# Optimization experiments

Measured on AMD Instinct MI355X. Metric: run time of the kernel, lower is better.

## Reference

```python
import jax, jax.numpy as jnp
import numpy as np

B, L, D, H = 2, 4096, 128, 4


def setup_inputs() -> dict:
    key = jax.random.key(0)
    k_x, k_q, k_k, k_v, k_o = jax.random.split(key, 5)
    std = 0.02
    x = jax.random.normal(k_x, (B, L, D), dtype=jnp.float32)
    # torch nn.Linear(d_model, H*d_model).weight has shape [H*D, D]
    Wq = std * jax.random.normal(k_q, (H * D, D), dtype=jnp.float32)
    Wk = std * jax.random.normal(k_k, (H * D, D), dtype=jnp.float32)
    Wv = std * jax.random.normal(k_v, (H * D, D), dtype=jnp.float32)
    # W_O: Linear(H*d_model, d_model).weight -> [D, H*D]
    Wo = std * jax.random.normal(k_o, (D, H * D), dtype=jnp.float32)
    return {"x": x, "Wq": Wq, "Wk": Wk, "Wv": Wv, "Wo": Wo}


def reference(x, Wq, Wk, Wv, Wo):
    # project: weight rows indexed by (h, e); out = x @ W^T
    Wq3 = Wq.reshape(H, D, D)
    Wk3 = Wk.reshape(H, D, D)
    Wv3 = Wv.reshape(H, D, D)
    q = jnp.einsum('bld,hed->bhle', x, Wq3)  # [B,H,L,D]
    k = jnp.einsum('bld,hed->bhle', x, Wk3)
    v = jnp.einsum('bld,hed->bhle', x, Wv3)
    logits = jnp.einsum('bhle,bhme->bhlm', q, k)  # [B,H,L,L]
    causal_mask = jnp.triu(jnp.ones((L, L), dtype=bool), 1)
    neg = jnp.finfo(logits.dtype).min
    logits = jnp.where(causal_mask, neg, logits)
    attn = jax.nn.softmax(logits, axis=-1)
    ctx = jnp.einsum('bhlm,bhme->bhle', attn, v)  # [B,H,L,D]
    ctx = ctx.transpose(0, 2, 1, 3).reshape(B, L, H * D)
    y = ctx @ Wo.T  # [B,L,D]
    return y
```

## Files before the change

### kernel.cpp

```cpp
#include <hip/hip_runtime.h>
#include <hip/hip_bf16.h>

#define BB 2
#define LL 4096
#define DD 128
#define HH 4

typedef unsigned short u16;
typedef unsigned int u32;
typedef __attribute__((ext_vector_type(8))) short short8;
typedef __attribute__((ext_vector_type(4))) float floatx4;

union PFrag { short8 s; u32 u[4]; };

__device__ __forceinline__ u16 f2bf(float f) {
    union { float f; u32 u; } v; v.f = f;
    return (u16)((v.u + 0x7fffu + ((v.u >> 16) & 1u)) >> 16);
}

__device__ __forceinline__ float bf2f(u16 u) {
    union { u32 u; float f; } v; v.u = (u32)u << 16;
    return v.f;
}

__device__ __forceinline__ u32 pk2bf(float a, float b) {
    union { __hip_bfloat162 h; u32 u; } v;
    v.h = __float22bfloat162_rn(float2{a, b});
    return v.u;
}

__device__ __forceinline__ void gld16(const u16* g, u16* l) {
    __builtin_amdgcn_global_load_lds((const __attribute__((address_space(1))) void*)g,
                                     (__attribute__((address_space(3))) void*)l, 16, 0, 0);
}

__device__ __forceinline__ int pfx2(int t) {
    int a = t >> 2, b = t & 3;
    return 2 * a * (a - 1) + a * b;
}

__device__ __forceinline__ void stage_tile_f32(const float* __restrict__ g,
                                               u16* lds, int tid) {
#pragma unroll
    for (int it = 0; it < 8; it++) {
        int unit = it * 256 + tid;
        int row = unit >> 4, uu = unit & 15;
        const float4* gp = (const float4*)(g + (size_t)row * 128 + uu * 8);
        float4 f0 = gp[0], f1 = gp[1];
        PFrag pv;
        pv.u[0] = pk2bf(f0.x, f0.y); pv.u[1] = pk2bf(f0.z, f0.w);
        pv.u[2] = pk2bf(f1.x, f1.y); pv.u[3] = pk2bf(f1.z, f1.w);
        *(short8*)(&lds[row * 128 + ((uu ^ (row & 15)) * 8)]) = pv.s;
    }
}

__global__ __launch_bounds__(256) void proj_qkv(const float* __restrict__ x,
                                                const float* __restrict__ wq,
                                                const float* __restrict__ wk,
                                                const float* __restrict__ wv,
                                                u16* __restrict__ Qb,
                                                u16* __restrict__ Kb,
                                                u16* __restrict__ Vt) {
    __shared__ __align__(16) u16 At[128 * 128];
    __shared__ __align__(16) u16 Wt[2][128 * 128];
    int tid  = threadIdx.x;
    int lane = tid & 63;
    int w    = tid >> 6;
    int c = lane & 15, g = lane >> 4;
    int mt = blockIdx.x;
    int h  = blockIdx.y;

    stage_tile_f32(x  + (size_t)mt * 128 * 128, At,    tid);
    stage_tile_f32(wq + (size_t)h  * 128 * 128, Wt[0], tid);
    __syncthreads();

#pragma unroll
    for (int z = 0; z < 3; z++) {
        if (z == 0) stage_tile_f32(wk + (size_t)h * 128 * 128, Wt[1], tid);
        if (z == 1) stage_tile_f32(wv + (size_t)h * 128 * 128, Wt[0], tid);
        const u16* Wcur = Wt[z & 1];
        const u16* Abuf = (z < 2) ? At : Wcur;
        const u16* Bbuf = (z < 2) ? Wcur : At;

        floatx4 acc[2][8];
#pragma unroll
        for (int m2 = 0; m2 < 2; m2++)
#pragma unroll
            for (int n2 = 0; n2 < 8; n2++) acc[m2][n2] = (floatx4){0.f, 0.f, 0.f, 0.f};

#pragma unroll
        for (int kk = 0; kk < 4; kk++) {
            short8 a0, a1, bf[8];
            {
                int r0 = w * 32 + c;
                int r1 = r0 + 16;
                a0 = *(const short8*)(&Abuf[r0 * 128 + (((g + 4 * kk) ^ (r0 & 15)) * 8)]);
                a1 = *(const short8*)(&Abuf[r1 * 128 + (((g + 4 * kk) ^ (r1 & 15)) * 8)]);
            }
#pragma unroll
            for (int n2 = 0; n2 < 8; n2++) {
                int rn = n2 * 16 + c;
                bf[n2] = *(const short8*)(&Bbuf[rn * 128 + (((g + 4 * kk) ^ (rn & 15)) * 8)]);
            }
#pragma unroll
            for (int n2 = 0; n2 < 8; n2++) {
                acc[0][n2] = __builtin_amdgcn_mfma_f32_16x16x32_bf16(a0, bf[n2], acc[0][n2], 0, 0, 0);
                acc[1][n2] = __builtin_amdgcn_mfma_f32_16x16x32_bf16(a1, bf[n2], acc[1][n2], 0, 0, 0);
            }
        }

        if (z < 2) {
            u16* out = (z == 0) ? Qb : Kb;
#pragma unroll
            for (int m2 = 0; m2 < 2; m2++)
#pragma unroll
                for (int r = 0; r < 4; r++) {
                    int lg = mt * 128 + w * 32 + m2 * 16 + g * 4 + r;
                    int b_ = lg >> 12, l = lg & 4095;
                    u16* op = out + ((size_t)(b_ * HH + h) * LL + l) * DD + c;
#pragma unroll
                    for (int n2 = 0; n2 < 8; n2++) op[n2 * 16] = f2bf(acc[m2][n2][r]);
                }
        } else {
            int b_ = mt >> 5;
            int lbase = (mt & 31) * 128;
#pragma unroll
            for (int m2 = 0; m2 < 2; m2++)
#pragma unroll
                for (int r = 0; r < 4; r++) {
                    int e = w * 32 + m2 * 16 + g * 4 + r;
                    u16* op = Vt + ((size_t)(b_ * HH + h) * DD + e) * LL + lbase + c;
#pragma unroll
                    for (int n2 = 0; n2 < 8; n2++) op[n2 * 16] = f2bf(acc[m2][n2][r]);
                }
        }
        __syncthreads();
    }
}

__global__ __launch_bounds__(256, 3) void flash_attn(const u16* __restrict__ Q,
                                                     const u16* __restrict__ K,
                                                     const u16* __restrict__ Vt,
                                                     u16* __restrict__ basep,
                                                     u16* __restrict__ slots,
                                                     float* __restrict__ l_acc) {
    __shared__ __align__(16) u16 Kls[2][32 * 128];
    __shared__ __align__(16) u16 Vls[2][512 * 8];

    int lane = threadIdx.x & 63;
    int w    = threadIdx.x >> 6;
    int c = lane & 15, g = lane >> 4;

    int bid  = blockIdx.x;
    int head = bid & 7;
    int i    = bid >> 3;
    int t, ch;
    if (i < 120) {
        int rem = i; ch = 0;
        while (rem >= 29 - 4 * ch) { rem -= 29 - 4 * ch; ch++; }
        t = 31 - rem;
    } else {
        int j = i - 120;
        if (j < 8)       { t = 30 - 4 * j;        ch = (t - 2) >> 2; }
        else if (j < 16) { t = 29 - 4 * (j - 8);  ch = (t - 1) >> 2; }
        else             { t = 28 - 4 * (j - 16); ch = t >> 2; }
    }

    int kstart = ch << 9;
    int kend   = min((t + 1) << 7, kstart + 512);
    int nsteps = (kend - kstart) >> 5;

    int qb = t * 128 + w * 32;
    int my_steps = min(nsteps, ((qb + 31 - kstart) >> 5) + 1);

    short8 bq0[4], bq1[4];
    {
        const u16* qp0 = Q + ((size_t)head * LL + qb + c) * DD + g * 8;
        const u16* qp1 = qp0 + 16 * DD;
#pragma unroll
        for (int kk = 0; kk < 4; kk++) {
            bq0[kk] = *(const short8*)(qp0 + kk * 32);
            bq1[kk] = *(const short8*)(qp1 + kk * 32);
        }
    }

    floatx4 o0[8], o1[8];
#pragma unroll
    for (int tt = 0; tt < 8; tt++) {
        o0[tt] = (floatx4){0.f, 0.f, 0.f, 0.f};
        o1[tt] = (floatx4){0.f, 0.f, 0.f, 0.f};
    }
    float lsum0 = 0.f, lsum1 = 0.f;

    int s0 = c + (((g << 1) & 3) << 4);
    int s1 = c + ((((g << 1) | 1) & 3) << 4);
    bool hi = (g >= 2);

    const u16* Kg0 = K  + ((size_t)head * LL + kstart) * DD;
    const u16* Vg0 = Vt + (size_t)head * DD * LL + kstart;

    int q0 = w * 64 + lane;
    int r0 = q0 >> 4, cc0 = (q0 & 15) ^ (r0 & 15);
    int r1 = r0 + 16,  cc1 = (q0 & 15) ^ (r1 & 15);
    int ve  = q0 & 127;
    int vka = (q0 >> 7) * 8;

#define STAGE(s) {                                                          \
        int buf_ = (s) & 1; int kb_ = (s) << 5;                             \
        const u16* Kg = Kg0 + (size_t)kb_ * DD;                             \
        const u16* Vg = Vg0 + kb_;                                          \
        gld16(Kg + r0 * DD + cc0 * 8, &Kls[buf_][w * 512]);                 \
        gld16(Kg + r1 * DD + cc1 * 8, &Kls[buf_][2048 + w * 512]);          \
        gld16(Vg + (size_t)ve * LL + vka,      &Vls[buf_][w * 512]);        \
        gld16(Vg + (size_t)ve * LL + vka + 16, &Vls[buf_][2048 + w * 512]); \
    }

    STAGE(0);

    for (int j = 0; j < nsteps; ++j) {
        __syncthreads();
        if (j + 1 < nsteps) STAGE(j + 1);
        if (j < my_steps) {
            int kb = kstart + (j << 5);
            const u16* Kb_ = &Kls[j & 1][0];
            const u16* Vb_ = &Vls[j & 1][0];

            floatx4 st00 = {0,0,0,0}, st01 = {0,0,0,0};
            floatx4 st10 = {0,0,0,0}, st11 = {0,0,0,0};
            {
                short8 ka[4];
#pragma unroll
                for (int kk = 0; kk < 4; kk++)
                    ka[kk] = *(const short8*)(Kb_ + c * 128 + (((g + 4 * kk) ^ c)) * 8);
#pragma unroll
                for (int kk = 0; kk < 4; kk++) {
                    st00 = __builtin_amdgcn_mfma_f32_16x16x32_bf16(ka[kk], bq0[kk], st00, 0, 0, 0);
                    st10 = __builtin_amdgcn_mfma_f32_16x16x32_bf16(ka[kk], bq1[kk], st10, 0, 0, 0);
                }
#pragma unroll
                for (int kk = 0; kk < 4; kk++)
                    ka[kk] = *(const short8*)(Kb_ + (16 + c) * 128 + (((g + 4 * kk) ^ c)) * 8);
#pragma unroll
                for (int kk = 0; kk < 4; kk++) {
                    st01 = __builtin_amdgcn_mfma_f32_16x16x32_bf16(ka[kk], bq0[kk], st01, 0, 0, 0);
                    st11 = __builtin_amdgcn_mfma_f32_16x16x32_bf16(ka[kk], bq1[kk], st11, 0, 0, 0);
                }
            }

            PFrag au0, au1;
#pragma unroll
            for (int qh = 0; qh < 2; qh++) {
                floatx4 sa = qh ? st10 : st00;
                floatx4 sb = qh ? st11 : st01;
                int qbh = qb + qh * 16;
                float p[8];
                if (kb + 31 > qbh) {
                    int q_c = qbh + c;
#pragma unroll
                    for (int r = 0; r < 4; r++) {
                        int k0 = kb + g * 4 + r;
                        p[r]     = (k0      <= q_c) ? sa[r] : -INFINITY;
                        p[4 + r] = (k0 + 16 <= q_c) ? sb[r] : -INFINITY;
                    }
                } else {
#pragma unroll
                    for (int r = 0; r < 4; r++) { p[r] = sa[r]; p[4 + r] = sb[r]; }
                }
                float ls = 0.f;
#pragma unroll
                for (int i2 = 0; i2 < 8; i2++) { p[i2] = __expf(p[i2]); ls += p[i2]; }
                if (qh) lsum1 += ls; else lsum0 += ls;

                u32 pk00 = pk2bf(p[0], p[1]);
                u32 pk01 = pk2bf(p[2], p[3]);
                u32 pk10 = pk2bf(p[4], p[5]);
                u32 pk11 = pk2bf(p[6], p[7]);
                u32 x00 = (u32)__shfl((int)pk00, s0), x10 = (u32)__shfl((int)pk10, s0);
                u32 x01 = (u32)__shfl((int)pk01, s0), x11 = (u32)__shfl((int)pk11, s0);
                u32 y00 = (u32)__shfl((int)pk00, s1), y10 = (u32)__shfl((int)pk10, s1);
                u32 y01 = (u32)__shfl((int)pk01, s1), y11 = (u32)__shfl((int)pk11, s1);
                PFrag* au = qh ? &au1 : &au0;
                au->u[0] = hi ? x10 : x00;
                au->u[1] = hi ? x11 : x01;
                au->u[2] = hi ? y10 : y00;
                au->u[3] = hi ? y11 : y01;
            }

#pragma unroll
            for (int tt = 0; tt < 8; tt++) {
                short8 vb = *(const short8*)(Vb_ + g * 1024 + tt * 128 + c * 8);
                o0[tt] = __builtin_amdgcn_mfma_f32_16x16x32_bf16(au0.s, vb, o0[tt], 0, 0, 0);
                o1[tt] = __builtin_amdgcn_mfma_f32_16x16x32_bf16(au1.s, vb, o1[tt], 0, 0, 0);
            }
        }
    }
#undef STAGE

    lsum0 += __shfl_xor(lsum0, 16); lsum0 += __shfl_xor(lsum0, 32);
    lsum1 += __shfl_xor(lsum1, 16); lsum1 += __shfl_xor(lsum1, 32);
    if (g == 0) {
        atomicAdd(&l_acc[head * LL + qb + c],      lsum0);
        atomicAdd(&l_acc[head * LL + qb + 16 + c], lsum1);
    }

    bool diag = (kstart + 512 >= ((t + 1) << 7));
    u16* dst0 = diag ? basep + ((size_t)head * LL + t * 128) * 128
                     : slots + ((size_t)(head * 112 + pfx2(t) + ch)) * 16384;
    dst0 += (size_t)(w * 32) * 128;
#pragma unroll
    for (int r = 0; r < 4; r++) {
        u16* d0 = dst0 + (g * 4 + r) * 128 + c;
        u16* d1 = d0 + 16 * 128;
#pragma unroll
        for (int tt = 0; tt < 8; tt++) {
            d0[tt * 16] = f2bf(o0[tt][r]);
            d1[tt * 16] = f2bf(o1[tt][r]);
        }
    }
}

__global__ __launch_bounds__(256) void norm_cast(const u16* __restrict__ basep,
                                                 const u16* __restrict__ slots,
                                                 const float* __restrict__ l_acc,
                                                 u16* __restrict__ ctx) {
    int i = blockIdx.x * 256 + threadIdx.x;
    int e4 = i * 4;
    int col = e4 & 511;
    int bl  = e4 >> 9;
    int b_ = bl >> 12, l = bl & 4095;
    int h = col >> 7, d = col & 127;
    int head = b_ * HH + h;
    int t = l >> 7;
    int nx = t >> 2;

    ushort4 bv = *(const ushort4*)(basep + ((size_t)head * LL + l) * 128 + d);
    float v0 = bf2f(bv.x), v1 = bf2f(bv.y), v2 = bf2f(bv.z), v3 = bf2f(bv.w);
    if (nx > 0) {
        int sb = head * 112 + pfx2(t);
        for (int x = 0; x < nx; x++) {
            ushort4 sv = *(const ushort4*)(slots + (size_t)(sb + x) * 16384 + (l & 127) * 128 + d);
            v0 += bf2f(sv.x); v1 += bf2f(sv.y); v2 += bf2f(sv.z); v3 += bf2f(sv.w);
        }
    }
    float inv = 1.f / l_acc[head * LL + l];
    ushort4 o;
    o.x = f2bf(v0 * inv); o.y = f2bf(v1 * inv);
    o.z = f2bf(v2 * inv); o.w = f2bf(v3 * inv);
    *(ushort4*)(ctx + e4) = o;
}

__global__ __launch_bounds__(256) void proj_out(const u16* __restrict__ ctx,
                                                const float* __restrict__ wo,
                                                float* __restrict__ y) {
    __shared__ __align__(16) u16 At[2][128 * 64];
    __shared__ __align__(16) u16 Wt[2][128 * 64];
    int tid  = threadIdx.x;
    int lane = tid & 63;
    int w    = tid >> 6;
    int c = lane & 15, g = lane >> 4;
    int mt = blockIdx.x;
    const u16* Ag = ctx + (size_t)mt * 128 * 512;

#define PSTAGE(kc) {                                                        \
        int buf_ = (kc) & 1; int ks_ = (kc) * 64;                           \
        _Pragma("unroll")                                                   \
        for (int i = 0; i < 4; i++) {                                       \
            int row = i * 32 + w * 8 + (lane >> 3);                         \
            int cc  = (lane & 7) ^ (row & 7);                               \
            gld16(Ag + (size_t)row * 512 + ks_ + cc * 8,                    \
                  &At[buf_][(i * 32 + w * 8) * 64]);                        \
        }                                                                   \
        _Pragma("unroll")                                                   \
        for (int it = 0; it < 4; it++) {                                    \
            int unit = it * 256 + tid;                                      \
            int row = unit >> 3, uu = unit & 7;                             \
            const float4* gp = (const float4*)(wo + (size_t)row * 512 +     \
                                               ks_ + uu * 8);               \
            float4 f0 = gp[0], f1 = gp[1];                                  \
            PFrag pv;                                                       \
            pv.u[0] = pk2bf(f0.x, f0.y); pv.u[1] = pk2bf(f0.z, f0.w);       \
            pv.u[2] = pk2bf(f1.x, f1.y); pv.u[3] = pk2bf(f1.z, f1.w);       \
            *(short8*)(&Wt[buf_][row * 64 + ((uu ^ (row & 7)) * 8)]) = pv.s;\
        }                                                                   \
    }

    floatx4 acc[2][8];
#pragma unroll
    for (int m2 = 0; m2 < 2; m2++)
#pragma unroll
        for (int n2 = 0; n2 < 8; n2++) acc[m2][n2] = (floatx4){0.f, 0.f, 0.f, 0.f};

    PSTAGE(0);
    for (int kc = 0; kc < 8; kc++) {
        __syncthreads();
        if (kc + 1 < 8) PSTAGE(kc + 1);
        int buf = kc & 1;
#pragma unroll
        for (int kk = 0; kk < 2; kk++) {
            int G = g + 4 * kk;
            short8 a0, a1, bf[8];
            {
                int ra = w * 32 + c;
                int rb = ra + 16;
                a0 = *(const short8*)(&At[buf][ra * 64 + ((G ^ (ra & 7)) * 8)]);
                a1 = *(const short8*)(&At[buf][rb * 64 + ((G ^ (rb & 7)) * 8)]);
            }
#pragma unroll
            for (int n2 = 0; n2 < 8; n2++) {
                int rn = n2 * 16 + c;
                bf[n2] = *(const short8*)(&Wt[buf][rn * 64 + ((G ^ (rn & 7)) * 8)]);
            }
#pragma unroll
            for (int n2 = 0; n2 < 8; n2++) {
                acc[0][n2] = __builtin_amdgcn_mfma_f32_16x16x32_bf16(a0, bf[n2], acc[0][n2], 0, 0, 0);
                acc[1][n2] = __builtin_amdgcn_mfma_f32_16x16x32_bf16(a1, bf[n2], acc[1][n2], 0, 0, 0);
            }
        }
    }
#undef PSTAGE

#pragma unroll
    for (int m2 = 0; m2 < 2; m2++)
#pragma unroll
        for (int r = 0; r < 4; r++) {
            int m = mt * 128 + w * 32 + m2 * 16 + g * 4 + r;
            float* yp = y + (size_t)m * 128 + c;
#pragma unroll
            for (int n2 = 0; n2 < 8; n2++) yp[n2 * 16] = acc[m2][n2][r];
        }
}

extern "C" void kernel_launch(void* const* d_in, const int* in_sizes, int n_in,
                              void* d_out, int out_size, void* d_ws, size_t ws_size,
                              hipStream_t stream) {
    const float* x  = (const float*)d_in[0];
    const float* Wq = (const float*)d_in[1];
    const float* Wk = (const float*)d_in[2];
    const float* Wv = (const float*)d_in[3];
    const float* Wo = (const float*)d_in[4];
    float* y = (float*)d_out;

    u16* ws  = (u16*)d_ws;
    u16* Qb  = ws;
    u16* Kb  = Qb + (size_t)BB * HH * LL * DD;
    u16* Vt  = Kb + (size_t)BB * HH * LL * DD;
    u16* ctx = Vt + (size_t)BB * HH * LL * DD;
    u16* basep = ctx + (size_t)BB * LL * HH * DD;
    u16* slots = basep + (size_t)8 * LL * 128;
    float* l_acc = (float*)(slots + (size_t)896 * 16384);

    (void)hipMemsetAsync(l_acc, 0, (size_t)8 * LL * 4, stream);

    proj_qkv<<<dim3(64, 4), 256, 0, stream>>>(x, Wq, Wk, Wv, Qb, Kb, Vt);
    flash_attn<<<dim3(1152), 256, 0, stream>>>(Qb, Kb, Vt, basep, slots, l_acc);
    norm_cast<<<dim3(4096), 256, 0, stream>>>(basep, slots, l_acc, ctx);
    proj_out<<<dim3(64), 256, 0, stream>>>(ctx, Wo, y);
}
```

Baseline: 153.6 us.

## Halve attention key-chunk size and proj_out row tile for more blocks

The flash-attention split-K chunk shrinks from 512 to 256 keys, raising the grid from 1152 to 2176 blocks. The slot indexing (pfxB), the diagonal test and the workspace size are updated to match. Separately, proj_out now uses 64-row tiles, giving 128 blocks instead of 64. Both changes aim to fill more CUs and balance the causal workload better. In exchange, norm_cast must read and sum twice as many bf16 partial slots per row, which adds memory traffic and per-block startup cost.

```diff
diff --git a/kernel.cpp b/kernel.cpp
--- a/kernel.cpp
+++ b/kernel.cpp
@@ -34,9 +34,9 @@
                                      (__attribute__((address_space(3))) void*)l, 16, 0, 0);
 }
 
-__device__ __forceinline__ int pfx2(int t) {
-    int a = t >> 2, b = t & 3;
-    return 2 * a * (a - 1) + a * b;
+__device__ __forceinline__ int pfxB(int t) {
+    int a = t >> 1, b = t & 1;
+    return a * (a - 1) + a * b;
 }
 
 __device__ __forceinline__ void stage_tile_f32(const float* __restrict__ g,
@@ -155,19 +155,17 @@
     int head = bid & 7;
     int i    = bid >> 3;
     int t, ch;
-    if (i < 120) {
-        int rem = i; ch = 0;
-        while (rem >= 29 - 4 * ch) { rem -= 29 - 4 * ch; ch++; }
-        t = 31 - rem;
+    if (i < 240) {
+        int rem = i; t = 31;
+        while (rem >= (t >> 1)) { rem -= (t >> 1); t--; }
+        ch = rem;
     } else {
-        int j = i - 120;
-        if (j < 8)       { t = 30 - 4 * j;        ch = (t - 2) >> 2; }
-        else if (j < 16) { t = 29 - 4 * (j - 8);  ch = (t - 1) >> 2; }
-        else             { t = 28 - 4 * (j - 16); ch = t >> 2; }
-    }
-
-    int kstart = ch << 9;
-    int kend   = min((t + 1) << 7, kstart + 512);
+        t = 31 - (i - 240);
+        ch = t >> 1;
+    }
+
+    int kstart = ch << 8;
+    int kend   = min((t + 1) << 7, kstart + 256);
     int nsteps = (kend - kstart) >> 5;
 
     int qb = t * 128 + w * 32;
@@ -303,9 +301,9 @@
         atomicAdd(&l_acc[head * LL + qb + 16 + c], lsum1);
     }
 
-    bool diag = (kstart + 512 >= ((t + 1) << 7));
+    bool diag = (ch == (t >> 1));
     u16* dst0 = diag ? basep + ((size_t)head * LL + t * 128) * 128
-                     : slots + ((size_t)(head * 112 + pfx2(t) + ch)) * 16384;
+                     : slots + ((size_t)(head * 240 + pfxB(t) + ch)) * 16384;
     dst0 += (size_t)(w * 32) * 128;
 #pragma unroll
     for (int r = 0; r < 4; r++) {
@@ -331,12 +329,12 @@
     int h = col >> 7, d = col & 127;
     int head = b_ * HH + h;
     int t = l >> 7;
-    int nx = t >> 2;
+    int nx = t >> 1;
 
     ushort4 bv = *(const ushort4*)(basep + ((size_t)head * LL + l) * 128 + d);
     float v0 = bf2f(bv.x), v1 = bf2f(bv.y), v2 = bf2f(bv.z), v3 = bf2f(bv.w);
     if (nx > 0) {
-        int sb = head * 112 + pfx2(t);
+        int sb = head * 240 + pfxB(t);
         for (int x = 0; x < nx; x++) {
             ushort4 sv = *(const ushort4*)(slots + (size_t)(sb + x) * 16384 + (l & 127) * 128 + d);
             v0 += bf2f(sv.x); v1 += bf2f(sv.y); v2 += bf2f(sv.z); v3 += bf2f(sv.w);
@@ -352,23 +350,24 @@
 __global__ __launch_bounds__(256) void proj_out(const u16* __restrict__ ctx,
                                                 const float* __restrict__ wo,
                                                 float* __restrict__ y) {
-    __shared__ __align__(16) u16 At[2][128 * 64];
+    __shared__ __align__(16) u16 At[2][64 * 64];
     __shared__ __align__(16) u16 Wt[2][128 * 64];
     int tid  = threadIdx.x;
     int lane = tid & 63;
     int w    = tid >> 6;
     int c = lane & 15, g = lane >> 4;
     int mt = blockIdx.x;
-    const u16* Ag = ctx + (size_t)mt * 128 * 512;
+    const u16* Ag = ctx + (size_t)mt * 64 * 512;
 
 #define PSTAGE(kc) {                                                        \
         int buf_ = (kc) & 1; int ks_ = (kc) * 64;                           \
         _Pragma("unroll")                                                   \
-        for (int i = 0; i < 4; i++) {                                       \
-            int row = i * 32 + w * 8 + (lane >> 3);                         \
-            int cc  = (lane & 7) ^ (row & 7);                               \
+        for (int it = 0; it < 2; it++) {                                    \
+            int unit = it * 256 + tid;                                      \
+            int row = unit >> 3, uu = unit & 7;                             \
+            int cc  = uu ^ (row & 7);                                       \
             gld16(Ag + (size_t)row * 512 + ks_ + cc * 8,                    \
-                  &At[buf_][(i * 32 + w * 8) * 64]);                        \
+                  &At[buf_][it * 2048 + w * 512]);                          \
         }                                                                   \
         _Pragma("unroll")                                                   \
         for (int it = 0; it < 4; it++) {                                    \
@@ -384,11 +383,9 @@
         }                                                                   \
     }
 
-    floatx4 acc[2][8];
-#pragma unroll
-    for (int m2 = 0; m2 < 2; m2++)
-#pragma unroll
-        for (int n2 = 0; n2 < 8; n2++) acc[m2][n2] = (floatx4){0.f, 0.f, 0.f, 0.f};
+    floatx4 acc[8];
+#pragma unroll
+    for (int n2 = 0; n2 < 8; n2++) acc[n2] = (floatx4){0.f, 0.f, 0.f, 0.f};
 
     PSTAGE(0);
     for (int kc = 0; kc < 8; kc++) {
@@ -398,12 +395,10 @@
 #pragma unroll
         for (int kk = 0; kk < 2; kk++) {
             int G = g + 4 * kk;
-            short8 a0, a1, bf[8];
+            short8 a0, bf[8];
             {
-                int ra = w * 32 + c;
-                int rb = ra + 16;
+                int ra = w * 16 + c;
                 a0 = *(const short8*)(&At[buf][ra * 64 + ((G ^ (ra & 7)) * 8)]);
-                a1 = *(const short8*)(&At[buf][rb * 64 + ((G ^ (rb & 7)) * 8)]);
             }
 #pragma unroll
             for (int n2 = 0; n2 < 8; n2++) {
@@ -411,23 +406,19 @@
                 bf[n2] = *(const short8*)(&Wt[buf][rn * 64 + ((G ^ (rn & 7)) * 8)]);
             }
 #pragma unroll
-            for (int n2 = 0; n2 < 8; n2++) {
-                acc[0][n2] = __builtin_amdgcn_mfma_f32_16x16x32_bf16(a0, bf[n2], acc[0][n2], 0, 0, 0);
-                acc[1][n2] = __builtin_amdgcn_mfma_f32_16x16x32_bf16(a1, bf[n2], acc[1][n2], 0, 0, 0);
-            }
+            for (int n2 = 0; n2 < 8; n2++)
+                acc[n2] = __builtin_amdgcn_mfma_f32_16x16x32_bf16(a0, bf[n2], acc[n2], 0, 0, 0);
         }
     }
 #undef PSTAGE
 
 #pragma unroll
-    for (int m2 = 0; m2 < 2; m2++)
-#pragma unroll
-        for (int r = 0; r < 4; r++) {
-            int m = mt * 128 + w * 32 + m2 * 16 + g * 4 + r;
-            float* yp = y + (size_t)m * 128 + c;
-#pragma unroll
-            for (int n2 = 0; n2 < 8; n2++) yp[n2 * 16] = acc[m2][n2][r];
-        }
+    for (int r = 0; r < 4; r++) {
+        int m = mt * 64 + w * 16 + g * 4 + r;
+        float* yp = y + (size_t)m * 128 + c;
+#pragma unroll
+        for (int n2 = 0; n2 < 8; n2++) yp[n2 * 16] = acc[n2][r];
+    }
 }
 
 extern "C" void kernel_launch(void* const* d_in, const int* in_sizes, int n_in,
@@ -447,12 +438,12 @@
     u16* ctx = Vt + (size_t)BB * HH * LL * DD;
     u16* basep = ctx + (size_t)BB * LL * HH * DD;
     u16* slots = basep + (size_t)8 * LL * 128;
-    float* l_acc = (float*)(slots + (size_t)896 * 16384);
+    float* l_acc = (float*)(slots + (size_t)1920 * 16384);
 
     (void)hipMemsetAsync(l_acc, 0, (size_t)8 * LL * 4, stream);
 
     proj_qkv<<<dim3(64, 4), 256, 0, stream>>>(x, Wq, Wk, Wv, Qb, Kb, Vt);
-    flash_attn<<<dim3(1152), 256, 0, stream>>>(Qb, Kb, Vt, basep, slots, l_acc);
+    flash_attn<<<dim3(2176), 256, 0, stream>>>(Qb, Kb, Vt, basep, slots, l_acc);
     norm_cast<<<dim3(4096), 256, 0, stream>>>(basep, slots, l_acc, ctx);
-    proj_out<<<dim3(64), 256, 0, stream>>>(ctx, Wo, y);
-}
+    proj_out<<<dim3(128), 256, 0, stream>>>(ctx, Wo, y);
+}
```

New measurement: 158.6 us. 1.03x slower.
